# Kernel tuning notes

Hardware: AMD Instinct MI355X
Metric: run time of the kernel (lower is better)

## Reference

```python
import jax, jax.numpy as jnp
import numpy as np


def setup_inputs() -> dict:
    key = jax.random.key(0)
    k1, k2, k3 = jax.random.split(key, 3)
    B, C, N, T = 32, 64, 1024, 64
    x = jax.random.normal(k1, (B, C, N, T), dtype=jnp.float32)
    W = jax.random.normal(k2, (T, T), dtype=jnp.float32) * 0.05
    alpha = jax.random.normal(k3, (C,), dtype=jnp.float32) * 0.1
    return {"x": x, "W": W, "alpha": alpha}


def reference(x, W, alpha):
    # x: [B, C, N, T]; channel-weighted reduction -> Q = K: [B, N, T]
    q = jnp.einsum('bcnt,c->bnt', x, alpha)
    # bilinear scores: K @ W @ Q^T -> [B, N, N]
    scores = jnp.einsum('bnt,ts,bms->bnm', q, W, q)
    return jax.nn.softmax(scores, axis=-1)
```

## Files before the change

kernel.cpp:

```cpp
#include <hip/hip_runtime.h>

#define B_ 32
#define C_ 64
#define N_ 1024
#define T_ 64

typedef __attribute__((ext_vector_type(8))) _Float16 half8;
typedef __attribute__((ext_vector_type(4))) _Float16 half4;
typedef __attribute__((ext_vector_type(4))) float f32x4;

__global__ __launch_bounds__(256) void k_q(const float* __restrict__ x,
                                           const float* __restrict__ alpha,
                                           _Float16* __restrict__ q_h) {
    const int bid = blockIdx.x;
    const int s1  = (bid & 7) * 256 + (bid >> 3);
    const int b   = s1 >> 6;
    const int n0  = (s1 & 63) * 16;
    const int tid = threadIdx.x;

    const f32x4* xb = (const f32x4*)(x + (size_t)b * C_ * N_ * T_
                                       + (size_t)n0 * T_);
    f32x4 acc = {0.f, 0.f, 0.f, 0.f};
#pragma unroll 4
    for (int c = 0; c < C_; ++c) {
        f32x4 v = __builtin_nontemporal_load(&xb[(size_t)c * (N_ * T_ / 4) + tid]);
        const float ac = alpha[c];
        acc[0] += ac * v[0]; acc[1] += ac * v[1];
        acc[2] += ac * v[2]; acc[3] += ac * v[3];
    }

    half4 h;
#pragma unroll
    for (int j = 0; j < 4; ++j) h[j] = (_Float16)acc[j];
    *(half4*)(q_h + ((size_t)b * N_ + n0) * T_ + (size_t)tid * 4) = h;
}

__global__ __launch_bounds__(512, 4) void k_scores_softmax(
        const _Float16* __restrict__ q_h,
        const float* __restrict__ W,
        float* __restrict__ out) {
    const int bid = blockIdx.x;
    const int s   = (bid & 7) * 128 + (bid >> 3);
    const int b   = s >> 5;
    const int n0  = (s & 31) * 32;
    const int tid  = threadIdx.x;
    const int w    = tid >> 6;
    const int lane = tid & 63;
    const int lr   = lane & 15;
    const int lk   = lane >> 4;

    __shared__ float Ws[T_][T_];
    __shared__ _Float16 qwh[32][72];
    __shared__ float red[32][8];

    {
        const f32x4* Wv = (const f32x4*)W;
        f32x4* Wd = (f32x4*)&Ws[0][0];
        Wd[tid]       = Wv[tid];
        Wd[tid + 512] = Wv[tid + 512];
    }
    __syncthreads();

    {
        const int tr = w >> 2, tc = w & 3;
        const size_t ar = ((size_t)b * N_ + n0 + tr * 16 + lr) * T_ + lk * 8;
        half8 a0 = *(const half8*)(q_h + ar);
        half8 a1 = *(const half8*)(q_h + ar + 32);
        half8 bh0, bh1, bl0, bl1;
#pragma unroll
        for (int j = 0; j < 8; ++j) {
            const float wv0 = Ws[lk * 8 + j][tc * 16 + lr];
            const float wv1 = Ws[lk * 8 + 32 + j][tc * 16 + lr];
            const _Float16 h0 = (_Float16)wv0;
            const _Float16 h1 = (_Float16)wv1;
            bh0[j] = h0; bl0[j] = (_Float16)(wv0 - (float)h0);
            bh1[j] = h1; bl1[j] = (_Float16)(wv1 - (float)h1);
        }
        f32x4 a = {0.f, 0.f, 0.f, 0.f};
        a = __builtin_amdgcn_mfma_f32_16x16x32_f16(a0, bh0, a, 0, 0, 0);
        a = __builtin_amdgcn_mfma_f32_16x16x32_f16(a1, bh1, a, 0, 0, 0);
        a = __builtin_amdgcn_mfma_f32_16x16x32_f16(a0, bl0, a, 0, 0, 0);
        a = __builtin_amdgcn_mfma_f32_16x16x32_f16(a1, bl1, a, 0, 0, 0);
#pragma unroll
        for (int r = 0; r < 4; ++r)
            qwh[tr * 16 + lk * 4 + r][tc * 16 + lr] = (_Float16)a[r];
    }
    __syncthreads();

    half8 af[2][2];
#pragma unroll
    for (int g = 0; g < 2; ++g) {
        af[g][0] = *(const half8*)&qwh[g * 16 + lr][lk * 8];
        af[g][1] = *(const half8*)&qwh[g * 16 + lr][lk * 8 + 32];
    }

    f32x4 acc[2][8];
#pragma unroll
    for (int g = 0; g < 2; ++g)
#pragma unroll
        for (int cf = 0; cf < 8; ++cf) acc[g][cf] = {0.f, 0.f, 0.f, 0.f};

    const size_t cb0 = ((size_t)b * N_ + w * 128 + lr) * T_ + lk * 8;
    half8 pb0 = *(const half8*)(q_h + cb0);
    half8 pb1 = *(const half8*)(q_h + cb0 + 32);
#pragma unroll
    for (int cf = 0; cf < 8; ++cf) {
        const half8 bh0 = pb0;
        const half8 bh1 = pb1;
        if (cf < 7) {
            const size_t cbn = cb0 + (size_t)(cf + 1) * 16 * T_;
            pb0 = *(const half8*)(q_h + cbn);
            pb1 = *(const half8*)(q_h + cbn + 32);
        }
#pragma unroll
        for (int g = 0; g < 2; ++g) {
            f32x4 a = acc[g][cf];
            a = __builtin_amdgcn_mfma_f32_16x16x32_f16(af[g][0], bh0, a, 0, 0, 0);
            a = __builtin_amdgcn_mfma_f32_16x16x32_f16(af[g][1], bh1, a, 0, 0, 0);
            acc[g][cf] = a;
        }
    }

    float sv[2][4];
#pragma unroll
    for (int g = 0; g < 2; ++g) {
#pragma unroll
        for (int r = 0; r < 4; ++r) {
            float ssum = 0.f;
#pragma unroll
            for (int cf = 0; cf < 8; ++cf) {
                float e = __expf(acc[g][cf][r]);
                acc[g][cf][r] = e;
                ssum += e;
            }
            ssum += __shfl_xor(ssum, 1);
            ssum += __shfl_xor(ssum, 2);
            ssum += __shfl_xor(ssum, 4);
            ssum += __shfl_xor(ssum, 8);
            sv[g][r] = ssum;
        }
        if (lr == 0) {
#pragma unroll
            for (int r = 0; r < 4; ++r) red[g * 16 + lk * 4 + r][w] = sv[g][r];
        }
    }
    __syncthreads();

#pragma unroll
    for (int g = 0; g < 2; ++g) {
#pragma unroll
        for (int r = 0; r < 4; ++r) {
            f32x4 p0 = *(f32x4*)&red[g * 16 + lk * 4 + r][0];
            f32x4 p1 = *(f32x4*)&red[g * 16 + lk * 4 + r][4];
            const float inv = 1.0f / (p0[0] + p0[1] + p0[2] + p0[3] +
                                      p1[0] + p1[1] + p1[2] + p1[3]);
            float* orow = out + ((size_t)b * N_ + n0 + g * 16 + lk * 4 + r) * N_
                              + w * 128 + lr;
#pragma unroll
            for (int cf = 0; cf < 8; ++cf)
                orow[cf * 16] = acc[g][cf][r] * inv;
        }
    }
}

extern "C" void kernel_launch(void* const* d_in, const int* in_sizes, int n_in,
                              void* d_out, int out_size, void* d_ws, size_t ws_size,
                              hipStream_t stream) {
    const float* x     = (const float*)d_in[0];
    const float* W     = (const float*)d_in[1];
    const float* alpha = (const float*)d_in[2];
    float* out = (float*)d_out;

    _Float16* q_h = (_Float16*)d_ws;

    k_q<<<2048, 256, 0, stream>>>(x, alpha, q_h);
    k_scores_softmax<<<1024, 512, 0, stream>>>(q_h, W, out);
}
```

Before: 125.0 us.

## Fuse q reduction and scores/softmax into one persistent producer-consumer kernel

The two launches are merged into one kernel of 512 blocks. Half the blocks produce the fp16 q for four batches each and publish completion through per-batch atomic flags. The other half wait on those flags and compute scores and softmax per batch, so reading x overlaps with writing the output. This relies on producer and consumer blocks being co-resident, since a spinning consumer could otherwise deadlock. It adds a flag-init launch and spin-wait overhead.

```diff
diff --git a/kernel.cpp b/kernel.cpp
--- a/kernel.cpp
+++ b/kernel.cpp
@@ -9,49 +9,64 @@
 typedef __attribute__((ext_vector_type(4))) _Float16 half4;
 typedef __attribute__((ext_vector_type(4))) float f32x4;
 
-__global__ __launch_bounds__(256) void k_q(const float* __restrict__ x,
-                                           const float* __restrict__ alpha,
-                                           _Float16* __restrict__ q_h) {
-    const int bid = blockIdx.x;
-    const int s1  = (bid & 7) * 256 + (bid >> 3);
-    const int b   = s1 >> 6;
-    const int n0  = (s1 & 63) * 16;
-    const int tid = threadIdx.x;
-
-    const f32x4* xb = (const f32x4*)(x + (size_t)b * C_ * N_ * T_
-                                       + (size_t)n0 * T_);
-    f32x4 acc = {0.f, 0.f, 0.f, 0.f};
-#pragma unroll 4
-    for (int c = 0; c < C_; ++c) {
-        f32x4 v = __builtin_nontemporal_load(&xb[(size_t)c * (N_ * T_ / 4) + tid]);
-        const float ac = alpha[c];
-        acc[0] += ac * v[0]; acc[1] += ac * v[1];
-        acc[2] += ac * v[2]; acc[3] += ac * v[3];
+
+__global__ void k_init(int* flags) {
+    if (threadIdx.x < 32) flags[threadIdx.x] = 0;
+}
+
+__global__ __launch_bounds__(512, 4) void k_fused(
+        const float* __restrict__ x,
+        const float* __restrict__ W,
+        const float* __restrict__ alpha,
+        float* __restrict__ out,
+        _Float16* __restrict__ q_h,
+        int* __restrict__ flags) {
+    const int u    = blockIdx.x;
+    const int xcd  = u & 7;
+    const int slot = u >> 3;
+    const int role = slot & 1;
+    const int m    = slot >> 1;
+    const int tid  = threadIdx.x;
+
+    __shared__ float Ws[T_][T_];
+    __shared__ _Float16 qwh[32][72];
+    __shared__ float red[32][8];
+
+    if (role) {
+        const int nr = m * 32;
+#pragma unroll 1
+        for (int g = 0; g < 4; ++g) {
+            const int b = g * 8 + xcd;
+            const float* xb = x + (size_t)b * C_ * N_ * T_ + (size_t)nr * T_;
+            f32x4 acc = {0.f, 0.f, 0.f, 0.f};
+#pragma unroll 8
+            for (int c = 0; c < C_; ++c) {
+                f32x4 v = __builtin_nontemporal_load(
+                    (const f32x4*)(xb + (size_t)c * N_ * T_) + tid);
+                const float ac = alpha[c];
+                acc[0] += ac * v[0]; acc[1] += ac * v[1];
+                acc[2] += ac * v[2]; acc[3] += ac * v[3];
+            }
+            half4 h;
+#pragma unroll
+            for (int j = 0; j < 4; ++j) h[j] = (_Float16)acc[j];
+            *(half4*)(q_h + ((size_t)b * N_ + nr) * T_ + (size_t)tid * 4) = h;
+
+            __syncthreads();
+            if (tid == 0) {
+                __threadfence();
+                __hip_atomic_fetch_add(&flags[g * 8 + xcd], 1,
+                                       __ATOMIC_RELEASE, __HIP_MEMORY_SCOPE_AGENT);
+            }
+        }
+        return;
     }
 
-    half4 h;
-#pragma unroll
-    for (int j = 0; j < 4; ++j) h[j] = (_Float16)acc[j];
-    *(half4*)(q_h + ((size_t)b * N_ + n0) * T_ + (size_t)tid * 4) = h;
-}
-
-__global__ __launch_bounds__(512, 4) void k_scores_softmax(
-        const _Float16* __restrict__ q_h,
-        const float* __restrict__ W,
-        float* __restrict__ out) {
-    const int bid = blockIdx.x;
-    const int s   = (bid & 7) * 128 + (bid >> 3);
-    const int b   = s >> 5;
-    const int n0  = (s & 31) * 32;
-    const int tid  = threadIdx.x;
     const int w    = tid >> 6;
     const int lane = tid & 63;
     const int lr   = lane & 15;
     const int lk   = lane >> 4;
-
-    __shared__ float Ws[T_][T_];
-    __shared__ _Float16 qwh[32][72];
-    __shared__ float red[32][8];
+    const int n0   = m * 32;
 
     {
         const f32x4* Wv = (const f32x4*)W;
@@ -61,105 +76,120 @@
     }
     __syncthreads();
 
-    {
-        const int tr = w >> 2, tc = w & 3;
-        const size_t ar = ((size_t)b * N_ + n0 + tr * 16 + lr) * T_ + lk * 8;
-        half8 a0 = *(const half8*)(q_h + ar);
-        half8 a1 = *(const half8*)(q_h + ar + 32);
-        half8 bh0, bh1, bl0, bl1;
-#pragma unroll
-        for (int j = 0; j < 8; ++j) {
-            const float wv0 = Ws[lk * 8 + j][tc * 16 + lr];
-            const float wv1 = Ws[lk * 8 + 32 + j][tc * 16 + lr];
-            const _Float16 h0 = (_Float16)wv0;
-            const _Float16 h1 = (_Float16)wv1;
-            bh0[j] = h0; bl0[j] = (_Float16)(wv0 - (float)h0);
-            bh1[j] = h1; bl1[j] = (_Float16)(wv1 - (float)h1);
-        }
-        f32x4 a = {0.f, 0.f, 0.f, 0.f};
-        a = __builtin_amdgcn_mfma_f32_16x16x32_f16(a0, bh0, a, 0, 0, 0);
-        a = __builtin_amdgcn_mfma_f32_16x16x32_f16(a1, bh1, a, 0, 0, 0);
-        a = __builtin_amdgcn_mfma_f32_16x16x32_f16(a0, bl0, a, 0, 0, 0);
-        a = __builtin_amdgcn_mfma_f32_16x16x32_f16(a1, bl1, a, 0, 0, 0);
-#pragma unroll
-        for (int r = 0; r < 4; ++r)
-            qwh[tr * 16 + lk * 4 + r][tc * 16 + lr] = (_Float16)a[r];
-    }
-    __syncthreads();
-
-    half8 af[2][2];
-#pragma unroll
-    for (int g = 0; g < 2; ++g) {
-        af[g][0] = *(const half8*)&qwh[g * 16 + lr][lk * 8];
-        af[g][1] = *(const half8*)&qwh[g * 16 + lr][lk * 8 + 32];
-    }
-
-    f32x4 acc[2][8];
-#pragma unroll
-    for (int g = 0; g < 2; ++g)
-#pragma unroll
-        for (int cf = 0; cf < 8; ++cf) acc[g][cf] = {0.f, 0.f, 0.f, 0.f};
-
-    const size_t cb0 = ((size_t)b * N_ + w * 128 + lr) * T_ + lk * 8;
-    half8 pb0 = *(const half8*)(q_h + cb0);
-    half8 pb1 = *(const half8*)(q_h + cb0 + 32);
-#pragma unroll
-    for (int cf = 0; cf < 8; ++cf) {
-        const half8 bh0 = pb0;
-        const half8 bh1 = pb1;
-        if (cf < 7) {
-            const size_t cbn = cb0 + (size_t)(cf + 1) * 16 * T_;
-            pb0 = *(const half8*)(q_h + cbn);
-            pb1 = *(const half8*)(q_h + cbn + 32);
-        }
-#pragma unroll
-        for (int g = 0; g < 2; ++g) {
-            f32x4 a = acc[g][cf];
-            a = __builtin_amdgcn_mfma_f32_16x16x32_f16(af[g][0], bh0, a, 0, 0, 0);
-            a = __builtin_amdgcn_mfma_f32_16x16x32_f16(af[g][1], bh1, a, 0, 0, 0);
-            acc[g][cf] = a;
-        }
-    }
-
-    float sv[2][4];
-#pragma unroll
-    for (int g = 0; g < 2; ++g) {
-#pragma unroll
-        for (int r = 0; r < 4; ++r) {
-            float ssum = 0.f;
-#pragma unroll
-            for (int cf = 0; cf < 8; ++cf) {
-                float e = __expf(acc[g][cf][r]);
-                acc[g][cf][r] = e;
-                ssum += e;
-            }
-            ssum += __shfl_xor(ssum, 1);
-            ssum += __shfl_xor(ssum, 2);
-            ssum += __shfl_xor(ssum, 4);
-            ssum += __shfl_xor(ssum, 8);
-            sv[g][r] = ssum;
-        }
-        if (lr == 0) {
-#pragma unroll
-            for (int r = 0; r < 4; ++r) red[g * 16 + lk * 4 + r][w] = sv[g][r];
-        }
-    }
-    __syncthreads();
-
-#pragma unroll
-    for (int g = 0; g < 2; ++g) {
-#pragma unroll
-        for (int r = 0; r < 4; ++r) {
-            f32x4 p0 = *(f32x4*)&red[g * 16 + lk * 4 + r][0];
-            f32x4 p1 = *(f32x4*)&red[g * 16 + lk * 4 + r][4];
-            const float inv = 1.0f / (p0[0] + p0[1] + p0[2] + p0[3] +
-                                      p1[0] + p1[1] + p1[2] + p1[3]);
-            float* orow = out + ((size_t)b * N_ + n0 + g * 16 + lk * 4 + r) * N_
-                              + w * 128 + lr;
-#pragma unroll
-            for (int cf = 0; cf < 8; ++cf)
-                orow[cf * 16] = acc[g][cf][r] * inv;
-        }
+#pragma unroll 1
+    for (int g = 0; g < 4; ++g) {
+        const int b = g * 8 + xcd;
+
+        if (tid == 0) {
+            while (__hip_atomic_load(&flags[g * 8 + xcd], __ATOMIC_RELAXED,
+                                     __HIP_MEMORY_SCOPE_AGENT) < 32)
+                __builtin_amdgcn_s_sleep(8);
+            __threadfence();
+        }
+        __syncthreads();
+
+        {
+            const int tr = w >> 2, tc = w & 3;
+            const size_t ar = ((size_t)b * N_ + n0 + tr * 16 + lr) * T_ + lk * 8;
+            half8 a0 = *(const half8*)(q_h + ar);
+            half8 a1 = *(const half8*)(q_h + ar + 32);
+            half8 bh0, bh1, bl0, bl1;
+#pragma unroll
+            for (int j = 0; j < 8; ++j) {
+                const float wv0 = Ws[lk * 8 + j][tc * 16 + lr];
+                const float wv1 = Ws[lk * 8 + 32 + j][tc * 16 + lr];
+                const _Float16 h0 = (_Float16)wv0;
+                const _Float16 h1 = (_Float16)wv1;
+                bh0[j] = h0; bl0[j] = (_Float16)(wv0 - (float)h0);
+                bh1[j] = h1; bl1[j] = (_Float16)(wv1 - (float)h1);
+            }
+            f32x4 a = {0.f, 0.f, 0.f, 0.f};
+            a = __builtin_amdgcn_mfma_f32_16x16x32_f16(a0, bh0, a, 0, 0, 0);
+            a = __builtin_amdgcn_mfma_f32_16x16x32_f16(a1, bh1, a, 0, 0, 0);
+            a = __builtin_amdgcn_mfma_f32_16x16x32_f16(a0, bl0, a, 0, 0, 0);
+            a = __builtin_amdgcn_mfma_f32_16x16x32_f16(a1, bl1, a, 0, 0, 0);
+#pragma unroll
+            for (int r = 0; r < 4; ++r)
+                qwh[tr * 16 + lk * 4 + r][tc * 16 + lr] = (_Float16)a[r];
+        }
+        __syncthreads();
+
+        half8 af[2][2];
+#pragma unroll
+        for (int gg = 0; gg < 2; ++gg) {
+            af[gg][0] = *(const half8*)&qwh[gg * 16 + lr][lk * 8];
+            af[gg][1] = *(const half8*)&qwh[gg * 16 + lr][lk * 8 + 32];
+        }
+
+        f32x4 acc[2][8];
+#pragma unroll
+        for (int gg = 0; gg < 2; ++gg)
+#pragma unroll
+            for (int cf = 0; cf < 8; ++cf) acc[gg][cf] = {0.f, 0.f, 0.f, 0.f};
+
+        const size_t cb0 = ((size_t)b * N_ + w * 128 + lr) * T_ + lk * 8;
+        half8 pb0 = *(const half8*)(q_h + cb0);
+        half8 pb1 = *(const half8*)(q_h + cb0 + 32);
+#pragma unroll
+        for (int cf = 0; cf < 8; ++cf) {
+            const half8 bh0 = pb0;
+            const half8 bh1 = pb1;
+            if (cf < 7) {
+                const size_t cbn = cb0 + (size_t)(cf + 1) * 16 * T_;
+                pb0 = *(const half8*)(q_h + cbn);
+                pb1 = *(const half8*)(q_h + cbn + 32);
+            }
+#pragma unroll
+            for (int gg = 0; gg < 2; ++gg) {
+                f32x4 a = acc[gg][cf];
+                a = __builtin_amdgcn_mfma_f32_16x16x32_f16(af[gg][0], bh0, a, 0, 0, 0);
+                a = __builtin_amdgcn_mfma_f32_16x16x32_f16(af[gg][1], bh1, a, 0, 0, 0);
+                acc[gg][cf] = a;
+            }
+        }
+
+        float sv[2][4];
+#pragma unroll
+        for (int gg = 0; gg < 2; ++gg) {
+#pragma unroll
+            for (int r = 0; r < 4; ++r) {
+                float ssum = 0.f;
+#pragma unroll
+                for (int cf = 0; cf < 8; ++cf) {
+                    float e = __expf(acc[gg][cf][r]);
+                    acc[gg][cf][r] = e;
+                    ssum += e;
+                }
+                ssum += __shfl_xor(ssum, 1);
+                ssum += __shfl_xor(ssum, 2);
+                ssum += __shfl_xor(ssum, 4);
+                ssum += __shfl_xor(ssum, 8);
+                sv[gg][r] = ssum;
+            }
+            if (lr == 0) {
+#pragma unroll
+                for (int r = 0; r < 4; ++r)
+                    red[gg * 16 + lk * 4 + r][w] = sv[gg][r];
+            }
+        }
+        __syncthreads();
+
+#pragma unroll
+        for (int gg = 0; gg < 2; ++gg) {
+#pragma unroll
+            for (int r = 0; r < 4; ++r) {
+                f32x4 p0 = *(f32x4*)&red[gg * 16 + lk * 4 + r][0];
+                f32x4 p1 = *(f32x4*)&red[gg * 16 + lk * 4 + r][4];
+                const float inv = 1.0f / (p0[0] + p0[1] + p0[2] + p0[3] +
+                                          p1[0] + p1[1] + p1[2] + p1[3]);
+                float* orow = out + ((size_t)b * N_ + n0 + gg * 16 + lk * 4 + r) * N_
+                                  + w * 128 + lr;
+#pragma unroll
+                for (int cf = 0; cf < 8; ++cf)
+                    orow[cf * 16] = acc[gg][cf][r] * inv;
+            }
+        }
+        __syncthreads();
     }
 }
 
@@ -172,7 +202,8 @@
     float* out = (float*)d_out;
 
     _Float16* q_h = (_Float16*)d_ws;
-
-    k_q<<<2048, 256, 0, stream>>>(x, alpha, q_h);
-    k_scores_softmax<<<1024, 512, 0, stream>>>(q_h, W, out);
+    int* flags    = (int*)((char*)d_ws + (4u << 20));
+
+    k_init<<<1, 32, 0, stream>>>(flags);
+    k_fused<<<512, 512, 0, stream>>>(x, W, alpha, out, q_h, flags);
 }
```

Measured after the change: 288.0 us. 130% more time.
